# Kernel tuning notes

Measured on AMD Instinct MI355X. Metric: run time of the kernel, lower is better.

## Reference

```python
import jax, jax.numpy as jnp
import numpy as np

N_HEAD = 16
N_KV_HEAD = 4
N_EMBD = 2048
HEAD_DIM = N_EMBD // N_HEAD  # 128
RMS_EPS = float(np.finfo(np.float32).eps)  # torch F.rms_norm default eps


def _apply_rotary(x, cos, sin):
    # x: [B,T,H,D]; cos/sin: [1,T,1,D/2]
    d = x.shape[-1] // 2
    x1, x2 = x[..., :d], x[..., d:]
    y1 = x1 * cos + x2 * sin
    y2 = -x1 * sin + x2 * cos
    return jnp.concatenate([y1, y2], axis=-1)


def _rms_norm(x):
    var = jnp.mean(jnp.square(x), axis=-1, keepdims=True)
    return x * jax.lax.rsqrt(var + RMS_EPS)


def setup_inputs() -> dict:
    key = jax.random.key(0)
    ks = jax.random.split(key, 7)
    B, T = 2, 2048
    x = jax.random.normal(ks[0], (B, T, N_EMBD), dtype=jnp.float32)
    cos = jax.random.normal(ks[1], (1, T, 1, HEAD_DIM // 2), dtype=jnp.float32)
    sin = jax.random.normal(ks[2], (1, T, 1, HEAD_DIM // 2), dtype=jnp.float32)
    s = 1.0 / np.sqrt(N_EMBD)
    Wq = jax.random.normal(ks[3], (N_HEAD * HEAD_DIM, N_EMBD), dtype=jnp.float32) * s
    Wk = jax.random.normal(ks[4], (N_KV_HEAD * HEAD_DIM, N_EMBD), dtype=jnp.float32) * s
    Wv = jax.random.normal(ks[5], (N_KV_HEAD * HEAD_DIM, N_EMBD), dtype=jnp.float32) * s
    Wo = jax.random.normal(ks[6], (N_EMBD, N_EMBD), dtype=jnp.float32) * s
    return {"x": x, "cos": cos, "sin": sin, "Wq": Wq, "Wk": Wk, "Wv": Wv, "Wo": Wo}


def reference(x, cos, sin, Wq, Wk, Wv, Wo):
    B, T, C = x.shape
    q = (x @ Wq.T).reshape(B, T, N_HEAD, HEAD_DIM)
    k = (x @ Wk.T).reshape(B, T, N_KV_HEAD, HEAD_DIM)
    v = (x @ Wv.T).reshape(B, T, N_KV_HEAD, HEAD_DIM)
    q = _rms_norm(_apply_rotary(q, cos, sin))
    k = _rms_norm(_apply_rotary(k, cos, sin))
    # to [B,H,T,D]; expand kv heads for GQA
    q = q.transpose(0, 2, 1, 3)
    k = k.transpose(0, 2, 1, 3)
    v = v.transpose(0, 2, 1, 3)
    g = N_HEAD // N_KV_HEAD
    k = jnp.repeat(k, g, axis=1)
    v = jnp.repeat(v, g, axis=1)
    scale = 1.0 / np.sqrt(HEAD_DIM)
    scores = jnp.einsum("bhtd,bhsd->bhts", q, k) * scale
    causal = jnp.tril(jnp.ones((T, T), dtype=bool))
    scores = jnp.where(causal, scores, -jnp.inf)
    attn = jax.nn.softmax(scores, axis=-1)
    y = jnp.einsum("bhts,bhsd->bhtd", attn, v)
    y = y.transpose(0, 2, 1, 3).reshape(B, T, C)
    return y @ Wo.T
```

## Files before the change

### kernel.cpp

```cpp
#include <hip/hip_runtime.h>
#include <hip/hip_bf16.h>
#include <stdint.h>

#define B_   2
#define T_   2048
#define CEMB 2048
#define H_   16
#define HKV_ 4
#define D_   128

typedef __attribute__((ext_vector_type(8))) short bf16x8;
typedef __attribute__((ext_vector_type(4))) float f32x4;
typedef __attribute__((ext_vector_type(16))) float f32x16;

#if __has_builtin(__builtin_amdgcn_exp2f)
#define EXP2(x) __builtin_amdgcn_exp2f(x)
#else
#define EXP2(x) exp2f(x)
#endif

__device__ __forceinline__ unsigned short f2b(float f) {
  union { float f; unsigned u; } v; v.f = f;
  unsigned r = v.u + 0x7FFFu + ((v.u >> 16) & 1u);
  return (unsigned short)(r >> 16);
}
__device__ __forceinline__ float b2f(unsigned short u) {
  union { unsigned u; float f; } v; v.u = ((unsigned)u) << 16; return v.f;
}
__device__ __forceinline__ unsigned cvtpk(float lo, float hi) {
  unsigned r;
  asm("v_cvt_pk_bf16_f32 %0, %1, %2" : "=v"(r) : "v"(lo), "v"(hi));
  return r;
}

#if __has_builtin(__builtin_amdgcn_permlane32_swap)
__device__ __forceinline__ void pl32(unsigned& a, unsigned& b) {
  auto r = __builtin_amdgcn_permlane32_swap(a, b, false, false);
  a = r[0]; b = r[1];
}
#else
__device__ __forceinline__ void pl32(unsigned& a, unsigned& b) {
  const bool hih = (threadIdx.x & 32) != 0;
  unsigned sa = __shfl_xor(a, 32), sb = __shfl_xor(b, 32);
  unsigned na = hih ? sb : a;
  unsigned nb = hih ? b : sa;
  a = na; b = nb;
}
#endif

__device__ __forceinline__ void gl16(const void* g, void* l) {
  __builtin_amdgcn_global_load_lds(
      (const __attribute__((address_space(1))) unsigned int*)g,
      (__attribute__((address_space(3))) unsigned int*)l, 16, 0, 0);
}

#define FENCE() asm volatile("" ::: "memory")

__global__ void cvt_kernel(const float* __restrict__ src,
                           unsigned short* __restrict__ dst, int n4) {
  int i = blockIdx.x * blockDim.x + threadIdx.x;
  const int stride = gridDim.x * blockDim.x;
  for (; i < n4; i += stride) {
    float4 v = ((const float4*)src)[i];
    ushort4 o;
    o.x = f2b(v.x); o.y = f2b(v.y); o.z = f2b(v.z); o.w = f2b(v.w);
    ((ushort4*)dst)[i] = o;
  }
}

__global__ __launch_bounds__(512, 2)
void gemm256(const unsigned short* __restrict__ A,
             const unsigned short* __restrict__ W,
             void* __restrict__ Cmat, int M, int N, int K, int obf16) {
  __shared__ alignas(16) unsigned short As[2][2][128][64];
  __shared__ alignas(16) unsigned short Bs[2][2][128][64];

  const int tid  = threadIdx.x;
  const int lane = tid & 63;
  const int w    = tid >> 6;
  const int wr   = w >> 2;
  const int wc   = w & 3;
  const int l16  = lane & 15, g4 = lane >> 4;
  const int srow = lane >> 3;
  const int schk = lane & 7;

  const int gx  = gridDim.x;
  const int nwg = gx * gridDim.y;
  const int lin = blockIdx.y * gx + blockIdx.x;
  const int cpx = nwg >> 3;
  const int swz = (lin & 7) * cpx + (lin >> 3);
  const int m0 = (swz / gx) * 256;
  const int n0 = (swz % gx) * 256;

  const unsigned short* Ap = A + (size_t)m0 * K;
  const unsigned short* Wp = W + (size_t)n0 * K;
  const int nk = K >> 6;

  f32x4 acc[8][4] = {};

  auto stA = [&](int ts, int h) {
    const unsigned short* g = Ap + (size_t)(h * 128 + w * 8 + srow) * K
                                 + ts * 64 + ((schk ^ srow) << 3);
    unsigned short* l = &As[ts & 1][h][w * 8][0];
    gl16(g, l);
    gl16(g + (size_t)64 * K, l + 64 * 64);
  };
  auto stB = [&](int ts, int h) {
    const unsigned short* g = Wp + (size_t)(h * 128 + w * 8 + srow) * K
                                 + ts * 64 + ((schk ^ srow) << 3);
    unsigned short* l = &Bs[ts & 1][h][w * 8][0];
    gl16(g, l);
    gl16(g + (size_t)64 * K, l + 64 * 64);
  };

  stA(0, 0); stB(0, 0); stA(0, 1); stB(0, 1);
  stA(1, 0); stB(1, 0);
  asm volatile("s_waitcnt vmcnt(4)" ::: "memory");
  __builtin_amdgcn_s_barrier();
  FENCE();

  for (int tau = 0; tau < nk; ++tau) {
    const int buf = tau & 1;
    bf16x8 af[4][2], bf0[2][2], bf1[2][2];
    #pragma unroll
    for (int mi = 0; mi < 4; ++mi) {
      const int har = (mi * 2 + wr) * 16 + l16;
      #pragma unroll
      for (int ks = 0; ks < 2; ++ks)
        af[mi][ks] = *(const bf16x8*)&As[buf][0][har][((ks * 4 + g4) ^ (l16 & 7)) << 3];
    }
    #pragma unroll
    for (int ni = 0; ni < 2; ++ni) {
      const int hbr = (ni * 4 + wc) * 16 + l16;
      #pragma unroll
      for (int ks = 0; ks < 2; ++ks)
        bf0[ni][ks] = *(const bf16x8*)&Bs[buf][0][hbr][((ks * 4 + g4) ^ (l16 & 7)) << 3];
    }
    if (tau + 1 < nk) stA(tau + 1, 1);
    __builtin_amdgcn_s_setprio(1);
    #pragma unroll
    for (int mi = 0; mi < 4; ++mi) {
      #pragma unroll
      for (int ni = 0; ni < 2; ++ni) {
        f32x4 t = acc[mi][ni];
        t = __builtin_amdgcn_mfma_f32_16x16x32_bf16(af[mi][0], bf0[ni][0], t, 0, 0, 0);
        t = __builtin_amdgcn_mfma_f32_16x16x32_bf16(af[mi][1], bf0[ni][1], t, 0, 0, 0);
        acc[mi][ni] = t;
      }
    }
    __builtin_amdgcn_s_setprio(0);
    __builtin_amdgcn_s_barrier();
    FENCE();
    #pragma unroll
    for (int ni = 0; ni < 2; ++ni) {
      const int hbr = (ni * 4 + wc) * 16 + l16;
      #pragma unroll
      for (int ks = 0; ks < 2; ++ks)
        bf1[ni][ks] = *(const bf16x8*)&Bs[buf][1][hbr][((ks * 4 + g4) ^ (l16 & 7)) << 3];
    }
    if (tau + 1 < nk) stB(tau + 1, 1);
    __builtin_amdgcn_s_setprio(1);
    #pragma unroll
    for (int mi = 0; mi < 4; ++mi) {
      #pragma unroll
      for (int ni = 0; ni < 2; ++ni) {
        f32x4 t = acc[mi][2 + ni];
        t = __builtin_amdgcn_mfma_f32_16x16x32_bf16(af[mi][0], bf1[ni][0], t, 0, 0, 0);
        t = __builtin_amdgcn_mfma_f32_16x16x32_bf16(af[mi][1], bf1[ni][1], t, 0, 0, 0);
        acc[mi][2 + ni] = t;
      }
    }
    __builtin_amdgcn_s_setprio(0);
    __builtin_amdgcn_s_barrier();
    FENCE();
    #pragma unroll
    for (int mi = 0; mi < 4; ++mi) {
      const int har = (mi * 2 + wr) * 16 + l16;
      #pragma unroll
      for (int ks = 0; ks < 2; ++ks)
        af[mi][ks] = *(const bf16x8*)&As[buf][1][har][((ks * 4 + g4) ^ (l16 & 7)) << 3];
    }
    if (tau + 2 < nk) stA(tau + 2, 0);
    __builtin_amdgcn_s_setprio(1);
    #pragma unroll
    for (int mi = 0; mi < 4; ++mi) {
      #pragma unroll
      for (int ni = 0; ni < 2; ++ni) {
        f32x4 t = acc[4 + mi][2 + ni];
        t = __builtin_amdgcn_mfma_f32_16x16x32_bf16(af[mi][0], bf1[ni][0], t, 0, 0, 0);
        t = __builtin_amdgcn_mfma_f32_16x16x32_bf16(af[mi][1], bf1[ni][1], t, 0, 0, 0);
        acc[4 + mi][2 + ni] = t;
      }
    }
    __builtin_amdgcn_s_setprio(0);
    __builtin_amdgcn_s_barrier();
    FENCE();
    if (tau + 2 < nk) stB(tau + 2, 0);
    __builtin_amdgcn_s_setprio(1);
    #pragma unroll
    for (int mi = 0; mi < 4; ++mi) {
      #pragma unroll
      for (int ni = 0; ni < 2; ++ni) {
        f32x4 t = acc[4 + mi][ni];
        t = __builtin_amdgcn_mfma_f32_16x16x32_bf16(af[mi][0], bf0[ni][0], t, 0, 0, 0);
        t = __builtin_amdgcn_mfma_f32_16x16x32_bf16(af[mi][1], bf0[ni][1], t, 0, 0, 0);
        acc[4 + mi][ni] = t;
      }
    }
    __builtin_amdgcn_s_setprio(0);
    if (tau + 2 < nk) asm volatile("s_waitcnt vmcnt(4)" ::: "memory");
    else              asm volatile("s_waitcnt vmcnt(0)" ::: "memory");
    __builtin_amdgcn_s_barrier();
    FENCE();
  }

  #pragma unroll
  for (int fr = 0; fr < 8; ++fr) {
    #pragma unroll
    for (int fc = 0; fc < 4; ++fc) {
      const int row = m0 + (fr * 2 + wr) * 16 + g4 * 4;
      const int col = n0 + (fc * 4 + wc) * 16 + l16;
      if (obf16) {
        unsigned short* Cb = (unsigned short*)Cmat;
        #pragma unroll
        for (int r = 0; r < 4; ++r)
          Cb[(size_t)(row + r) * N + col] = f2b(acc[fr][fc][r]);
      } else {
        float* Cf = (float*)Cmat;
        #pragma unroll
        for (int r = 0; r < 4; ++r)
          Cf[(size_t)(row + r) * N + col] = acc[fr][fc][r];
      }
    }
  }
}

__global__ __launch_bounds__(512, 2)
void gemm_n128(const unsigned short* __restrict__ A,
               const unsigned short* __restrict__ W,
               float* __restrict__ Cmat, int M, int N, int K) {
  __shared__ alignas(16) unsigned short As[2][2][128][64];
  __shared__ alignas(16) unsigned short Bs[2][2][64][64];

  const int tid  = threadIdx.x;
  const int lane = tid & 63;
  const int w    = tid >> 6;
  const int wr   = w >> 2;
  const int wc   = w & 3;
  const int l16  = lane & 15, g4 = lane >> 4;
  const int srow = lane >> 3;
  const int schk = lane & 7;

  const int gx  = gridDim.x;
  const int nwg = gx * gridDim.y;
  const int lin = blockIdx.y * gx + blockIdx.x;
  const int cpx = nwg >> 3;
  const int swz = (lin & 7) * cpx + (lin >> 3);
  const int m0 = (swz / gx) * 256;
  const int n0 = (swz % gx) * 128;

  const unsigned short* Ap = A + (size_t)m0 * K;
  const unsigned short* Wp = W + (size_t)n0 * K;
  const int nk = K >> 6;

  const int bh_ = wc >> 1;
  const int br0 = (wc & 1) * 32;

  f32x4 acc[8][2] = {};

  auto stA = [&](int ts, int h) {
    const unsigned short* g = Ap + (size_t)(h * 128 + w * 8 + srow) * K
                                 + ts * 64 + ((schk ^ srow) << 3);
    unsigned short* l = &As[ts & 1][h][w * 8][0];
    gl16(g, l);
    gl16(g + (size_t)64 * K, l + 64 * 64);
  };
  auto stB = [&](int ts, int h) {
    const unsigned short* g = Wp + (size_t)(h * 64 + w * 8 + srow) * K
                                 + ts * 64 + ((schk ^ srow) << 3);
    gl16(g, &Bs[ts & 1][h][w * 8][0]);
  };

  stA(0, 0); stA(0, 1); stB(0, 0); stB(0, 1);
  stA(1, 0); stB(1, 0); stB(1, 1);
  asm volatile("s_waitcnt vmcnt(4)" ::: "memory");
  __builtin_amdgcn_s_barrier();
  FENCE();

  for (int t = 0; t < nk; ++t) {
    const int buf = t & 1;
    bf16x8 af[4][2], bfr[2][2];
    #pragma unroll
    for (int mi = 0; mi < 4; ++mi) {
      const int har = (mi * 2 + wr) * 16 + l16;
      #pragma unroll
      for (int ks = 0; ks < 2; ++ks)
        af[mi][ks] = *(const bf16x8*)&As[buf][0][har][((ks * 4 + g4) ^ (l16 & 7)) << 3];
    }
    #pragma unroll
    for (int fc = 0; fc < 2; ++fc) {
      const int br = br0 + fc * 16 + l16;
      #pragma unroll
      for (int ks = 0; ks < 2; ++ks)
        bfr[fc][ks] = *(const bf16x8*)&Bs[buf][bh_][br][((ks * 4 + g4) ^ (l16 & 7)) << 3];
    }
    if (t + 1 < nk) stA(t + 1, 1);
    __builtin_amdgcn_s_setprio(1);
    #pragma unroll
    for (int mi = 0; mi < 4; ++mi) {
      #pragma unroll
      for (int fc = 0; fc < 2; ++fc) {
        f32x4 a = acc[mi][fc];
        a = __builtin_amdgcn_mfma_f32_16x16x32_bf16(af[mi][0], bfr[fc][0], a, 0, 0, 0);
        a = __builtin_amdgcn_mfma_f32_16x16x32_bf16(af[mi][1], bfr[fc][1], a, 0, 0, 0);
        acc[mi][fc] = a;
      }
    }
    __builtin_amdgcn_s_setprio(0);
    if (t + 2 < nk) asm volatile("s_waitcnt vmcnt(6)" ::: "memory");
    else            asm volatile("s_waitcnt vmcnt(0)" ::: "memory");
    __builtin_amdgcn_s_barrier();
    FENCE();
    #pragma unroll
    for (int mi = 0; mi < 4; ++mi) {
      const int har = (mi * 2 + wr) * 16 + l16;
      #pragma unroll
      for (int ks = 0; ks < 2; ++ks)
        af[mi][ks] = *(const bf16x8*)&As[buf][1][har][((ks * 4 + g4) ^ (l16 & 7)) << 3];
    }
    if (t + 2 < nk) { stA(t + 2, 0); stB(t + 2, 0); stB(t + 2, 1); }
    __builtin_amdgcn_s_setprio(1);
    #pragma unroll
    for (int mi = 0; mi < 4; ++mi) {
      #pragma unroll
      for (int fc = 0; fc < 2; ++fc) {
        f32x4 a = acc[4 + mi][fc];
        a = __builtin_amdgcn_mfma_f32_16x16x32_bf16(af[mi][0], bfr[fc][0], a, 0, 0, 0);
        a = __builtin_amdgcn_mfma_f32_16x16x32_bf16(af[mi][1], bfr[fc][1], a, 0, 0, 0);
        acc[4 + mi][fc] = a;
      }
    }
    __builtin_amdgcn_s_setprio(0);
    if (t + 2 < nk) asm volatile("s_waitcnt vmcnt(6)" ::: "memory");
    else            asm volatile("s_waitcnt vmcnt(0)" ::: "memory");
    __builtin_amdgcn_s_barrier();
    FENCE();
  }

  #pragma unroll
  for (int fr = 0; fr < 8; ++fr) {
    const int hh = fr >> 2, mi = fr & 3;
    #pragma unroll
    for (int fc = 0; fc < 2; ++fc) {
      const int row = m0 + hh * 128 + (mi * 2 + wr) * 16 + g4 * 4;
      const int col = n0 + wc * 32 + fc * 16 + l16;
      #pragma unroll
      for (int r = 0; r < 4; ++r)
        Cmat[(size_t)(row + r) * N + col] = acc[fr][fc][r];
    }
  }
}

__global__ __launch_bounds__(128)
void rope_norm(const unsigned short* __restrict__ X, int rstride,
               const float* __restrict__ Cos, const float* __restrict__ Sin,
               unsigned short* __restrict__ Out, int Hn, float out_scale) {
  const int idx = blockIdx.x;
  const int h  = idx % Hn;
  const int bt = idx / Hn;
  const int t  = bt & (T_ - 1);
  const int b  = bt >> 11;
  const int d  = threadIdx.x;
  const unsigned short* src = X + (size_t)bt * rstride + h * D_;
  float y;
  if (d < 64) {
    float x1 = b2f(src[d]), x2 = b2f(src[d + 64]);
    float c = Cos[t * 64 + d], s = Sin[t * 64 + d];
    y = x1 * c + x2 * s;
  } else {
    int dd = d - 64;
    float x1 = b2f(src[dd]), x2 = b2f(src[d]);
    float c = Cos[t * 64 + dd], s = Sin[t * 64 + dd];
    y = -x1 * s + x2 * c;
  }
  float ss = y * y;
  #pragma unroll
  for (int m = 32; m; m >>= 1) ss += __shfl_xor(ss, m);
  __shared__ float red[2];
  if ((d & 63) == 0) red[d >> 6] = ss;
  __syncthreads();
  const float tot  = red[0] + red[1];
  const float rinv = rsqrtf(tot * (1.0f / 128.0f) + 1.1920929e-7f) * out_scale;
  Out[(((size_t)b * Hn + h) * T_ + t) * D_ + d] = f2b(y * rinv);
}

__global__ __launch_bounds__(256)
void vtrans(const unsigned short* __restrict__ Vf, int rstride,
            unsigned short* __restrict__ Vt) {
  __shared__ float tile[32][65];
  const int t0 = blockIdx.x * 64;
  const int d0 = blockIdx.y * 32;
  const int bh = blockIdx.z;
  const int b = bh >> 2, hk = bh & 3;
  const int tid = threadIdx.x;
  {
    const int di = tid & 31, ts = tid >> 5;
    #pragma unroll
    for (int i = 0; i < 8; ++i) {
      int tt = ts + i * 8;
      tile[di][tt] = b2f(Vf[(size_t)(b * T_ + t0 + tt) * rstride + hk * D_ + d0 + di]);
    }
  }
  __syncthreads();
  {
    const int ti = tid & 63, ds = tid >> 6;
    #pragma unroll
    for (int i = 0; i < 8; ++i) {
      int dd = ds * 8 + i;
      Vt[((size_t)bh * D_ + d0 + dd) * T_ + t0 + ti] = f2b(tile[dd][ti]);
    }
  }
}

#define KVB 128

__global__ __launch_bounds__(512)
void attn_kernel(const unsigned short* __restrict__ Qn,
                 const unsigned short* __restrict__ Kn,
                 const unsigned short* __restrict__ Vt,
                 unsigned short* __restrict__ Yb) {
  __shared__ alignas(16) unsigned short Ks[2][KVB][D_];
  __shared__ alignas(16) unsigned short Vs[2][D_][KVB];

  const int tid = threadIdx.x;
  const int lane = tid & 63;
  const int w = tid >> 6;
  const int wq  = w & 3;
  const int kvg = w >> 2;
  const int l31 = lane & 31;
  const int hi  = lane >> 5;
  const int bh = blockIdx.x;
  const int by = blockIdx.y;
  const int qt = (by < 8) ? by : 23 - by;
  const int b = bh >> 4, h = bh & 15;
  const int hk = h >> 2;

  const unsigned short* kp = Kn + ((size_t)(b * HKV_ + hk) * T_) * D_;
  const unsigned short* vp = Vt + ((size_t)(b * HKV_ + hk) * D_) * T_;

  const int r4 = lane >> 4, c16 = lane & 15;

  const int t0 = qt * 128;
  const int qrow0 = t0 + wq * 32;
  const int qmax = qrow0 + 31;
  const int nt = qt + 1;
  const int qglob = qrow0 + l31;

  const unsigned short* qp = Qn + ((size_t)bh * T_ + qrow0) * D_;
  bf16x8 qf[8];
  #pragma unroll
  for (int ds = 0; ds < 8; ++ds)
    qf[ds] = *(const bf16x8*)(qp + (size_t)l31 * D_ + ds * 16 + hi * 8);

  f32x16 o[4] = {};
  float l_lane = 0.f;

  auto stage = [&](int tt) {
    const int buf = tt & 1;
    const int kv = tt * KVB;
    #pragma unroll
    for (int j = 0; j < 4; ++j) {
      const int row = w * 16 + j * 4 + r4;
      const int cg = c16 ^ (row & 7);
      gl16(kp + (size_t)(kv + row) * D_ + cg * 8, &Ks[buf][w * 16 + j * 4][0]);
    }
    #pragma unroll
    for (int j = 0; j < 4; ++j) {
      const int row = w * 16 + j * 4 + r4;
      const int cg = c16 ^ (row & 7);
      gl16(vp + (size_t)row * T_ + kv + cg * 8, &Vs[buf][w * 16 + j * 4][0]);
    }
  };

  stage(0);

  union PAu { unsigned u[4]; bf16x8 v; };

  for (int t = 0; t < nt; ++t) {
    __syncthreads();
    if (t + 1 < nt) stage(t + 1);
    const int kbase = t * KVB + kvg * 64;
    if (kbase <= qmax) {
      const unsigned short (*kb)[D_]  = Ks[t & 1];
      const unsigned short (*vbp)[KVB] = Vs[t & 1];
      f32x16 s0 = {}, s1 = {};
      #pragma unroll
      for (int ds = 0; ds < 8; ++ds) {
        const int key0 = kvg * 64 + l31;
        const int key1 = kvg * 64 + 32 + l31;
        bf16x8 k0 = *(const bf16x8*)&kb[key0][(((ds * 2 + hi) ^ (key0 & 7)) << 3)];
        bf16x8 k1 = *(const bf16x8*)&kb[key1][(((ds * 2 + hi) ^ (key1 & 7)) << 3)];
        s0 = __builtin_amdgcn_mfma_f32_32x32x16_bf16(k0, qf[ds], s0, 0, 0, 0);
        s1 = __builtin_amdgcn_mfma_f32_32x32x16_bf16(k1, qf[ds], s1, 0, 0, 0);
      }
      const bool need_mask = (kbase + 63 > qrow0);
      float e0[16], e1[16];
      float ls = 0.f;
      #pragma unroll
      for (int r = 0; r < 16; ++r) {
        const int crow = (r & 3) + 8 * (r >> 2) + 4 * hi;
        float v0 = EXP2(s0[r]);
        float v1 = EXP2(s1[r]);
        if (need_mask) {
          v0 = (kbase + crow      <= qglob) ? v0 : 0.f;
          v1 = (kbase + 32 + crow <= qglob) ? v1 : 0.f;
        }
        e0[r] = v0; e1[r] = v1;
        ls += v0 + v1;
      }
      l_lane += ls;
      PAu pa[4];
      {
        unsigned a0 = cvtpk(e0[0],  e0[1]),  a1 = cvtpk(e0[2],  e0[3]);
        unsigned b0 = cvtpk(e0[4],  e0[5]),  b1 = cvtpk(e0[6],  e0[7]);
        unsigned c0 = cvtpk(e0[8],  e0[9]),  c1 = cvtpk(e0[10], e0[11]);
        unsigned d0 = cvtpk(e0[12], e0[13]), d1 = cvtpk(e0[14], e0[15]);
        pl32(a0, b0); pl32(a1, b1); pl32(c0, d0); pl32(c1, d1);
        pa[0].u[0] = a0; pa[0].u[1] = a1; pa[0].u[2] = b0; pa[0].u[3] = b1;
        pa[1].u[0] = c0; pa[1].u[1] = c1; pa[1].u[2] = d0; pa[1].u[3] = d1;
      }
      {
        unsigned a0 = cvtpk(e1[0],  e1[1]),  a1 = cvtpk(e1[2],  e1[3]);
        unsigned b0 = cvtpk(e1[4],  e1[5]),  b1 = cvtpk(e1[6],  e1[7]);
        unsigned c0 = cvtpk(e1[8],  e1[9]),  c1 = cvtpk(e1[10], e1[11]);
        unsigned d0 = cvtpk(e1[12], e1[13]), d1 = cvtpk(e1[14], e1[15]);
        pl32(a0, b0); pl32(a1, b1); pl32(c0, d0); pl32(c1, d1);
        pa[2].u[0] = a0; pa[2].u[1] = a1; pa[2].u[2] = b0; pa[2].u[3] = b1;
        pa[3].u[0] = c0; pa[3].u[1] = c1; pa[3].u[2] = d0; pa[3].u[3] = d1;
      }
      #pragma unroll
      for (int ks = 0; ks < 4; ++ks) {
        #pragma unroll
        for (int db = 0; db < 4; ++db) {
          const int d = db * 32 + l31;
          const int c = (kvg * 8 + ks * 2 + hi) ^ (d & 7);
          bf16x8 vf = *(const bf16x8*)&vbp[d][c << 3];
          o[db] = __builtin_amdgcn_mfma_f32_32x32x16_bf16(pa[ks].v, vf, o[db], 0, 0, 0);
        }
      }
    }
  }

  const float lfull = l_lane + __shfl_xor(l_lane, 32);
  __syncthreads();
  float* obuf = (float*)&Ks[0][0][0];
  float* lbuf = (float*)&Vs[0][0][0];
  if (w >= 4) {
    const int base = (w - 4) * 4096;
    #pragma unroll
    for (int r = 0; r < 16; ++r)
      #pragma unroll
      for (int db = 0; db < 4; ++db)
        obuf[base + (r * 4 + db) * 64 + lane] = o[db][r];
    if (hi == 0) lbuf[(w - 4) * 32 + l31] = lfull;
  }
  __syncthreads();
  if (w < 4) {
    const int base = w * 4096;
    const float ltot = lfull + lbuf[w * 32 + l31];
    const float invq = 1.0f / ltot;
    #pragma unroll
    for (int r = 0; r < 16; ++r) {
      const int crow = (r & 3) + 8 * (r >> 2) + 4 * hi;
      const float inv = __shfl(invq, crow);
      unsigned short* yrow = Yb + ((size_t)(b * T_ + qrow0 + crow) * CEMB) + h * D_;
      #pragma unroll
      for (int db = 0; db < 4; ++db)
        yrow[db * 32 + l31] = f2b((o[db][r] + obuf[base + (r * 4 + db) * 64 + lane]) * inv);
    }
  }
}

extern "C" void kernel_launch(void* const* d_in, const int* in_sizes, int n_in,
                              void* d_out, int out_size, void* d_ws, size_t ws_size,
                              hipStream_t stream) {
  const float* x    = (const float*)d_in[0];
  const float* cosp = (const float*)d_in[1];
  const float* sinp = (const float*)d_in[2];
  const float* Wq   = (const float*)d_in[3];
  const float* Wk   = (const float*)d_in[4];
  const float* Wv   = (const float*)d_in[5];
  const float* Wo   = (const float*)d_in[6];
  float* out = (float*)d_out;

  char* ws = (char*)d_ws;
  size_t off = 0;
  auto alloc = [&](size_t bytes) {
    void* p = ws + off;
    off += (bytes + 255) & ~(size_t)255;
    return p;
  };
  const size_t MT = (size_t)B_ * T_;
  const int NQKV = 3072;
  unsigned short* xb    = (unsigned short*)alloc(MT * CEMB * 2);
  unsigned short* wqkvb = (unsigned short*)alloc((size_t)NQKV * 2048 * 2);
  unsigned short* wob   = (unsigned short*)alloc((size_t)2048 * 2048 * 2);
  unsigned short* qkvb  = (unsigned short*)alloc(MT * NQKV * 2);
  unsigned short* qn    = (unsigned short*)alloc((size_t)B_ * H_ * T_ * D_ * 2);
  unsigned short* kn    = (unsigned short*)alloc((size_t)B_ * HKV_ * T_ * D_ * 2);
  unsigned short* vt    = (unsigned short*)alloc((size_t)B_ * HKV_ * D_ * T_ * 2);
  unsigned short* yb    = (unsigned short*)alloc(MT * CEMB * 2);

  cvt_kernel<<<2048, 256, 0, stream>>>(x,  xb, (int)(MT * CEMB / 4));
  cvt_kernel<<<1024, 256, 0, stream>>>(Wq, wqkvb,                2048 * 2048 / 4);
  cvt_kernel<<<256,  256, 0, stream>>>(Wk, wqkvb + 2048 * 2048,  512 * 2048 / 4);
  cvt_kernel<<<256,  256, 0, stream>>>(Wv, wqkvb + 2560 * 2048,  512 * 2048 / 4);
  cvt_kernel<<<1024, 256, 0, stream>>>(Wo, wob,                  2048 * 2048 / 4);

  gemm256<<<dim3(NQKV / 256, 4096 / 256), 512, 0, stream>>>(xb, wqkvb, qkvb, 4096, NQKV, 2048, 1);

  rope_norm<<<4096 * H_,   128, 0, stream>>>(qkvb,        NQKV, cosp, sinp, qn, H_,   0.1275174324f);
  rope_norm<<<4096 * HKV_, 128, 0, stream>>>(qkvb + 2048, NQKV, cosp, sinp, kn, HKV_, 1.0f);
  vtrans<<<dim3(T_ / 64, D_ / 32, B_ * HKV_), 256, 0, stream>>>(qkvb + 2560, NQKV, vt);

  attn_kernel<<<dim3(B_ * H_, 16), 512, 0, stream>>>(qn, kn, vt, yb);

  gemm_n128<<<dim3(2048 / 128, 4096 / 256), 512, 0, stream>>>(yb, wob, out, 4096, 2048, 2048);
}
```

Baseline: 203.0 us.

## Retile QKV GEMM to 256x192 tiles and raise MFMA priority in attention

The QKV projection GEMM changes from 256x256 tiles to 256x192. The grid grows from 12x16=192 to 16x16=256 workgroups, which should fill the 256 CUs better. The main loop is restructured from four phases into two, with a single full B tile per stage and new vmcnt waits. The attention kernel also wraps its QK and PV MFMA loops in s_setprio(1) so the matrix work gets scheduling priority. The cost is less reuse per tile and a different load/wait schedule, which could expose more memory latency.

```diff
diff --git a/kernel.cpp b/kernel.cpp
--- a/kernel.cpp
+++ b/kernel.cpp
@@ -69,11 +69,11 @@
 }
 
 __global__ __launch_bounds__(512, 2)
-void gemm256(const unsigned short* __restrict__ A,
-             const unsigned short* __restrict__ W,
-             void* __restrict__ Cmat, int M, int N, int K, int obf16) {
+void gemm_n192(const unsigned short* __restrict__ A,
+               const unsigned short* __restrict__ W,
+               unsigned short* __restrict__ Cmat, int M, int N, int K) {
   __shared__ alignas(16) unsigned short As[2][2][128][64];
-  __shared__ alignas(16) unsigned short Bs[2][2][128][64];
+  __shared__ alignas(16) unsigned short Bs[2][192][64];
 
   const int tid  = threadIdx.x;
   const int lane = tid & 63;
@@ -90,13 +90,13 @@
   const int cpx = nwg >> 3;
   const int swz = (lin & 7) * cpx + (lin >> 3);
   const int m0 = (swz / gx) * 256;
-  const int n0 = (swz % gx) * 256;
+  const int n0 = (swz % gx) * 192;
 
   const unsigned short* Ap = A + (size_t)m0 * K;
   const unsigned short* Wp = W + (size_t)n0 * K;
   const int nk = K >> 6;
 
-  f32x4 acc[8][4] = {};
+  f32x4 acc[8][3] = {};
 
   auto stA = [&](int ts, int h) {
     const unsigned short* g = Ap + (size_t)(h * 128 + w * 8 + srow) * K
@@ -105,23 +105,21 @@
     gl16(g, l);
     gl16(g + (size_t)64 * K, l + 64 * 64);
   };
-  auto stB = [&](int ts, int h) {
-    const unsigned short* g = Wp + (size_t)(h * 128 + w * 8 + srow) * K
+  auto stB = [&](int ts, int j) {
+    const unsigned short* g = Wp + (size_t)(j * 64 + w * 8 + srow) * K
                                  + ts * 64 + ((schk ^ srow) << 3);
-    unsigned short* l = &Bs[ts & 1][h][w * 8][0];
-    gl16(g, l);
-    gl16(g + (size_t)64 * K, l + 64 * 64);
+    gl16(g, &Bs[ts & 1][j * 64 + w * 8][0]);
   };
 
-  stA(0, 0); stB(0, 0); stA(0, 1); stB(0, 1);
-  stA(1, 0); stB(1, 0);
-  asm volatile("s_waitcnt vmcnt(4)" ::: "memory");
+  stA(0, 0); stA(0, 1); stB(0, 0); stB(0, 1); stB(0, 2);
+  stA(1, 0); stB(1, 0); stB(1, 1); stB(1, 2);
+  asm volatile("s_waitcnt vmcnt(5)" ::: "memory");
   __builtin_amdgcn_s_barrier();
   FENCE();
 
-  for (int tau = 0; tau < nk; ++tau) {
-    const int buf = tau & 1;
-    bf16x8 af[4][2], bf0[2][2], bf1[2][2];
+  for (int t = 0; t < nk; ++t) {
+    const int buf = t & 1;
+    bf16x8 af[4][2], bfr[3][2];
     #pragma unroll
     for (int mi = 0; mi < 4; ++mi) {
       const int har = (mi * 2 + wr) * 16 + l16;
@@ -130,107 +128,65 @@
         af[mi][ks] = *(const bf16x8*)&As[buf][0][har][((ks * 4 + g4) ^ (l16 & 7)) << 3];
     }
     #pragma unroll
-    for (int ni = 0; ni < 2; ++ni) {
-      const int hbr = (ni * 4 + wc) * 16 + l16;
+    for (int fc = 0; fc < 3; ++fc) {
+      const int br = wc * 48 + fc * 16 + l16;
       #pragma unroll
       for (int ks = 0; ks < 2; ++ks)
-        bf0[ni][ks] = *(const bf16x8*)&Bs[buf][0][hbr][((ks * 4 + g4) ^ (l16 & 7)) << 3];
-    }
-    if (tau + 1 < nk) stA(tau + 1, 1);
+        bfr[fc][ks] = *(const bf16x8*)&Bs[buf][br][((ks * 4 + g4) ^ (l16 & 7)) << 3];
+    }
+    if (t + 1 < nk) stA(t + 1, 1);
     __builtin_amdgcn_s_setprio(1);
     #pragma unroll
     for (int mi = 0; mi < 4; ++mi) {
       #pragma unroll
-      for (int ni = 0; ni < 2; ++ni) {
-        f32x4 t = acc[mi][ni];
-        t = __builtin_amdgcn_mfma_f32_16x16x32_bf16(af[mi][0], bf0[ni][0], t, 0, 0, 0);
-        t = __builtin_amdgcn_mfma_f32_16x16x32_bf16(af[mi][1], bf0[ni][1], t, 0, 0, 0);
-        acc[mi][ni] = t;
+      for (int fc = 0; fc < 3; ++fc) {
+        f32x4 a = acc[mi][fc];
+        a = __builtin_amdgcn_mfma_f32_16x16x32_bf16(af[mi][0], bfr[fc][0], a, 0, 0, 0);
+        a = __builtin_amdgcn_mfma_f32_16x16x32_bf16(af[mi][1], bfr[fc][1], a, 0, 0, 0);
+        acc[mi][fc] = a;
       }
     }
     __builtin_amdgcn_s_setprio(0);
+    if (t + 2 < nk) asm volatile("s_waitcnt vmcnt(7)" ::: "memory");
+    else            asm volatile("s_waitcnt vmcnt(0)" ::: "memory");
     __builtin_amdgcn_s_barrier();
     FENCE();
     #pragma unroll
-    for (int ni = 0; ni < 2; ++ni) {
-      const int hbr = (ni * 4 + wc) * 16 + l16;
+    for (int mi = 0; mi < 4; ++mi) {
+      const int har = (mi * 2 + wr) * 16 + l16;
       #pragma unroll
       for (int ks = 0; ks < 2; ++ks)
-        bf1[ni][ks] = *(const bf16x8*)&Bs[buf][1][hbr][((ks * 4 + g4) ^ (l16 & 7)) << 3];
-    }
-    if (tau + 1 < nk) stB(tau + 1, 1);
+        af[mi][ks] = *(const bf16x8*)&As[buf][1][har][((ks * 4 + g4) ^ (l16 & 7)) << 3];
+    }
+    if (t + 2 < nk) { stA(t + 2, 0); stB(t + 2, 0); stB(t + 2, 1); stB(t + 2, 2); }
     __builtin_amdgcn_s_setprio(1);
     #pragma unroll
     for (int mi = 0; mi < 4; ++mi) {
       #pragma unroll
-      for (int ni = 0; ni < 2; ++ni) {
-        f32x4 t = acc[mi][2 + ni];
-        t = __builtin_amdgcn_mfma_f32_16x16x32_bf16(af[mi][0], bf1[ni][0], t, 0, 0, 0);
-        t = __builtin_amdgcn_mfma_f32_16x16x32_bf16(af[mi][1], bf1[ni][1], t, 0, 0, 0);
-        acc[mi][2 + ni] = t;
+      for (int fc = 0; fc < 3; ++fc) {
+        f32x4 a = acc[4 + mi][fc];
+        a = __builtin_amdgcn_mfma_f32_16x16x32_bf16(af[mi][0], bfr[fc][0], a, 0, 0, 0);
+        a = __builtin_amdgcn_mfma_f32_16x16x32_bf16(af[mi][1], bfr[fc][1], a, 0, 0, 0);
+        acc[4 + mi][fc] = a;
       }
     }
     __builtin_amdgcn_s_setprio(0);
+    if (t + 2 < nk) asm volatile("s_waitcnt vmcnt(7)" ::: "memory");
+    else            asm volatile("s_waitcnt vmcnt(0)" ::: "memory");
     __builtin_amdgcn_s_barrier();
     FENCE();
-    #pragma unroll
-    for (int mi = 0; mi < 4; ++mi) {
-      const int har = (mi * 2 + wr) * 16 + l16;
-      #pragma unroll
-      for (int ks = 0; ks < 2; ++ks)
-        af[mi][ks] = *(const bf16x8*)&As[buf][1][har][((ks * 4 + g4) ^ (l16 & 7)) << 3];
-    }
-    if (tau + 2 < nk) stA(tau + 2, 0);
-    __builtin_amdgcn_s_setprio(1);
-    #pragma unroll
-    for (int mi = 0; mi < 4; ++mi) {
-      #pragma unroll
-      for (int ni = 0; ni < 2; ++ni) {
-        f32x4 t = acc[4 + mi][2 + ni];
-        t = __builtin_amdgcn_mfma_f32_16x16x32_bf16(af[mi][0], bf1[ni][0], t, 0, 0, 0);
-        t = __builtin_amdgcn_mfma_f32_16x16x32_bf16(af[mi][1], bf1[ni][1], t, 0, 0, 0);
-        acc[4 + mi][2 + ni] = t;
-      }
-    }
-    __builtin_amdgcn_s_setprio(0);
-    __builtin_amdgcn_s_barrier();
-    FENCE();
-    if (tau + 2 < nk) stB(tau + 2, 0);
-    __builtin_amdgcn_s_setprio(1);
-    #pragma unroll
-    for (int mi = 0; mi < 4; ++mi) {
-      #pragma unroll
-      for (int ni = 0; ni < 2; ++ni) {
-        f32x4 t = acc[4 + mi][ni];
-        t = __builtin_amdgcn_mfma_f32_16x16x32_bf16(af[mi][0], bf0[ni][0], t, 0, 0, 0);
-        t = __builtin_amdgcn_mfma_f32_16x16x32_bf16(af[mi][1], bf0[ni][1], t, 0, 0, 0);
-        acc[4 + mi][ni] = t;
-      }
-    }
-    __builtin_amdgcn_s_setprio(0);
-    if (tau + 2 < nk) asm volatile("s_waitcnt vmcnt(4)" ::: "memory");
-    else              asm volatile("s_waitcnt vmcnt(0)" ::: "memory");
-    __builtin_amdgcn_s_barrier();
-    FENCE();
   }
 
   #pragma unroll
   for (int fr = 0; fr < 8; ++fr) {
-    #pragma unroll
-    for (int fc = 0; fc < 4; ++fc) {
-      const int row = m0 + (fr * 2 + wr) * 16 + g4 * 4;
-      const int col = n0 + (fc * 4 + wc) * 16 + l16;
-      if (obf16) {
-        unsigned short* Cb = (unsigned short*)Cmat;
-        #pragma unroll
-        for (int r = 0; r < 4; ++r)
-          Cb[(size_t)(row + r) * N + col] = f2b(acc[fr][fc][r]);
-      } else {
-        float* Cf = (float*)Cmat;
-        #pragma unroll
-        for (int r = 0; r < 4; ++r)
-          Cf[(size_t)(row + r) * N + col] = acc[fr][fc][r];
-      }
+    const int hh = fr >> 2, mi = fr & 3;
+    #pragma unroll
+    for (int fc = 0; fc < 3; ++fc) {
+      const int row = m0 + hh * 128 + (mi * 2 + wr) * 16 + g4 * 4;
+      const int col = n0 + wc * 48 + fc * 16 + l16;
+      #pragma unroll
+      for (int r = 0; r < 4; ++r)
+        Cmat[(size_t)(row + r) * N + col] = f2b(acc[fr][fc][r]);
     }
   }
 }
@@ -494,6 +450,7 @@
       const unsigned short (*kb)[D_]  = Ks[t & 1];
       const unsigned short (*vbp)[KVB] = Vs[t & 1];
       f32x16 s0 = {}, s1 = {};
+      __builtin_amdgcn_s_setprio(1);
       #pragma unroll
       for (int ds = 0; ds < 8; ++ds) {
         const int key0 = kvg * 64 + l31;
@@ -503,6 +460,7 @@
         s0 = __builtin_amdgcn_mfma_f32_32x32x16_bf16(k0, qf[ds], s0, 0, 0, 0);
         s1 = __builtin_amdgcn_mfma_f32_32x32x16_bf16(k1, qf[ds], s1, 0, 0, 0);
       }
+      __builtin_amdgcn_s_setprio(0);
       const bool need_mask = (kbase + 63 > qrow0);
       float e0[16], e1[16];
       float ls = 0.f;
@@ -538,6 +496,7 @@
         pa[2].u[0] = a0; pa[2].u[1] = a1; pa[2].u[2] = b0; pa[2].u[3] = b1;
         pa[3].u[0] = c0; pa[3].u[1] = c1; pa[3].u[2] = d0; pa[3].u[3] = d1;
       }
+      __builtin_amdgcn_s_setprio(1);
       #pragma unroll
       for (int ks = 0; ks < 4; ++ks) {
         #pragma unroll
@@ -548,6 +507,7 @@
           o[db] = __builtin_amdgcn_mfma_f32_32x32x16_bf16(pa[ks].v, vf, o[db], 0, 0, 0);
         }
       }
+      __builtin_amdgcn_s_setprio(0);
     }
   }
 
@@ -617,7 +577,7 @@
   cvt_kernel<<<256,  256, 0, stream>>>(Wv, wqkvb + 2560 * 2048,  512 * 2048 / 4);
   cvt_kernel<<<1024, 256, 0, stream>>>(Wo, wob,                  2048 * 2048 / 4);
 
-  gemm256<<<dim3(NQKV / 256, 4096 / 256), 512, 0, stream>>>(xb, wqkvb, qkvb, 4096, NQKV, 2048, 1);
+  gemm_n192<<<dim3(NQKV / 192, 4096 / 256), 512, 0, stream>>>(xb, wqkvb, qkvb, 4096, NQKV, 2048);
 
   rope_norm<<<4096 * H_,   128, 0, stream>>>(qkvb,        NQKV, cosp, sinp, qn, H_,   0.1275174324f);
   rope_norm<<<4096 * HKV_, 128, 0, stream>>>(qkvb + 2048, NQKV, cosp, sinp, kn, HKV_, 1.0f);
```

Result: faster. 197.1 us (-2.9%).
